# Optimization experiments

Measured on AMD Instinct MI355X. Metric: run time of the kernel, lower is better.

## Reference

```python
import jax, jax.numpy as jnp
import numpy as np

BETA = 0.9      # LIF leak factor
THR = 1.0       # firing threshold
SLOPE = 5.0     # surrogate-gradient sigmoid slope


def spike_fn(v):
    # Heaviside forward, sigmoid surrogate gradient (straight-through).
    hard = (v > THR).astype(v.dtype)
    surr = jax.nn.sigmoid(SLOPE * (v - THR))
    return hard + (surr - jax.lax.stop_gradient(surr))


def setup_inputs() -> dict:
    key = jax.random.key(0)
    ks = jax.random.split(key, 4)
    B, T, IN, H, OUT = 16, 128, 1024, 4096, 1024
    def lin_w(k, out_d, in_d):
        bound = 1.0 / np.sqrt(in_d)
        return jax.random.uniform(k, (out_d, in_d), jnp.float32, -bound, bound)
    return {
        "x": jax.random.normal(ks[0], (B, T, IN), jnp.float32),
        "w1": lin_w(ks[1], H, IN), "b1": jnp.zeros((H,), jnp.float32),
        "w2": lin_w(ks[2], H, H),  "b2": jnp.zeros((H,), jnp.float32),
        "w3": lin_w(ks[3], OUT, H), "b3": jnp.zeros((OUT,), jnp.float32),
    }


def reference(x, w1, b1, w2, b2, w3, b3):
    # x: [B, T, IN]; sequential per-timestep SNN feed-forward, readout = sum over time.
    B = x.shape[0]
    H = w1.shape[0]
    v0 = jnp.zeros((B, H), x.dtype)

    def step(carry, xt):                      # xt: [B, IN]
        v1, v2 = carry
        h1 = xt @ w1.T + b1                   # [B, H]
        v1 = BETA * v1 + h1
        s1 = spike_fn(v1)
        v1 = v1 - s1 * THR                    # soft reset
        h2 = s1 @ w2.T + b2                   # [B, H]
        v2 = BETA * v2 + h2
        s2 = spike_fn(v2)
        v2 = v2 - s2 * THR
        logits = s2 @ w3.T + b3               # [B, OUT]
        return (v1, v2), logits

    _, logits = jax.lax.scan(step, (v0, v0), jnp.swapaxes(x, 0, 1))  # [T, B, OUT]
    return logits.sum(axis=0)                 # readout_mode == 'sum'
```

## Files before the change

### kernel.cpp

```cpp
#include <hip/hip_runtime.h>
#include <hip/hip_bf16.h>

#define B_   16
#define T_   128
#define IN_  1024
#define H_   4096
#define OUT_ 1024
#define M_   (B_ * T_)

typedef __attribute__((ext_vector_type(8))) short short8;
typedef __attribute__((ext_vector_type(4))) float f32x4;
typedef __attribute__((ext_vector_type(4))) int i32x4;
typedef __attribute__((ext_vector_type(4))) unsigned short u16x4;
typedef unsigned short u16;
typedef signed char i8;

__device__ inline u16 f2bf_rne(float f) {
  unsigned u = __float_as_uint(f);
  unsigned r = u + 0x7FFFu + ((u >> 16) & 1u);
  return (u16)(r >> 16);
}
__device__ inline float bf2f(u16 s) {
  return __uint_as_float(((unsigned)s) << 16);
}
__device__ inline int pack4(int a, int b, int c, int d) {
  return (a & 255) | ((b & 255) << 8) | ((c & 255) << 16) | ((d & 255) << 24);
}

__device__ inline void xcd_swizzle(int bid0, int& bnI, int& bmI) {
  const int xcd = bid0 & 7;
  const int loc = bid0 >> 3;
  bnI = (xcd & 3) * 8 + (loc & 7);
  bmI = (xcd >> 2) * 8 + (loc >> 3);
}

#define NX_  (M_ * IN_)
#define NW1_ (H_ * IN_)
#define NW2_ (H_ * H_)

__device__ inline void split4bf(const float4 f, u16* __restrict__ hi,
                                u16* __restrict__ lo, size_t e) {
  u16x4 h, l;
  h.x = f2bf_rne(f.x); l.x = f2bf_rne(f.x - bf2f(h.x));
  h.y = f2bf_rne(f.y); l.y = f2bf_rne(f.y - bf2f(h.y));
  h.z = f2bf_rne(f.z); l.z = f2bf_rne(f.z - bf2f(h.z));
  h.w = f2bf_rne(f.w); l.w = f2bf_rne(f.w - bf2f(h.w));
  *(u16x4*)(hi + e) = h;
  *(u16x4*)(lo + e) = l;
}

__device__ inline void splitw2_1(float w, int& c0, int& c1, int& c2) {
  int wf = __float2int_rn(w * 268435456.0f);
  c0 = (wf + 32768) >> 16;
  int r0 = wf - (c0 << 16);
  if (r0 >= 32640) { c0 += 1; r0 -= 65536; }
  c1 = (r0 + 128) >> 8;
  c2 = r0 - (c1 << 8);
}

__global__ void split_xw1_kernel(const float4* __restrict__ x,
                                 const float4* __restrict__ w1,
                                 u16* __restrict__ xh, u16* __restrict__ xl,
                                 u16* __restrict__ w1h, u16* __restrict__ w1l) {
  const int total4 = (NX_ + NW1_) / 4;
  for (int i = blockIdx.x * blockDim.x + threadIdx.x; i < total4;
       i += gridDim.x * blockDim.x) {
    if (i < NX_ / 4) {
      split4bf(x[i], xh, xl, (size_t)i * 4);
    } else {
      int j = i - NX_ / 4;
      split4bf(w1[j], w1h, w1l, (size_t)j * 4);
    }
  }
}

#define BK1 64

__global__ __launch_bounds__(256, 2) void gemm1_rec(
    const u16* __restrict__ Ah, const u16* __restrict__ Al,
    const u16* __restrict__ Bh, const u16* __restrict__ Bl,
    const float* __restrict__ bias, i8* __restrict__ s1out,
    const float4* __restrict__ w2src,
    i8* __restrict__ p0, i8* __restrict__ p1, i8* __restrict__ p2) {
  __shared__ __align__(16) char smem[65536];
  u16* sAh = (u16*)smem;
  u16* sAl = (u16*)(smem + 16384);
  u16* sBh = (u16*)(smem + 32768);
  u16* sBl = (u16*)(smem + 49152);

  const int tid  = threadIdx.x;
  const int lane = tid & 63;
  const int wid  = tid >> 6;
  const int wm   = (wid >> 1) * 64;
  const int wn   = (wid & 1) * 64;
  const int bid  = blockIdx.y * 32 + blockIdx.x;
  int bnI, bmI;
  xcd_swizzle(bid, bnI, bmI);
  const int bm = bmI * 128;
  const int bn = bnI * 128;

  const int sdst = (tid & 7) * 8;
  const int scol = (((tid & 7) ^ ((tid >> 3) & 7)) * 8);
  const int q8   = (lane >> 4) * 8;
  const int rsw  = (lane & 7) * 8;

  f32x4 acc[4][4];
#pragma unroll
  for (int i = 0; i < 4; ++i)
#pragma unroll
    for (int j = 0; j < 4; ++j) acc[i][j] = (f32x4){0.f, 0.f, 0.f, 0.f};

  const int wbase = bid * 8192 + tid * 2;
  float4 wfa = w2src[wbase];
  float4 wfb = w2src[wbase + 1];

#pragma unroll 1
  for (int it = 0; it < IN_ / BK1; ++it) {
    const int kt = it * BK1;
    __syncthreads();
#pragma unroll
    for (int l = 0; l < 4; ++l) {
      int row = l * 32 + (tid >> 3);
      size_t ga = (size_t)(bm + row) * IN_ + kt + scol;
      size_t gb = (size_t)(bn + row) * IN_ + kt + scol;
      int ld = row * BK1 + sdst;
      __builtin_amdgcn_global_load_lds(
          (const __attribute__((address_space(1))) unsigned int*)(Ah + ga),
          (__attribute__((address_space(3))) unsigned int*)(&sAh[ld]), 16, 0, 0);
      __builtin_amdgcn_global_load_lds(
          (const __attribute__((address_space(1))) unsigned int*)(Al + ga),
          (__attribute__((address_space(3))) unsigned int*)(&sAl[ld]), 16, 0, 0);
      __builtin_amdgcn_global_load_lds(
          (const __attribute__((address_space(1))) unsigned int*)(Bh + gb),
          (__attribute__((address_space(3))) unsigned int*)(&sBh[ld]), 16, 0, 0);
      __builtin_amdgcn_global_load_lds(
          (const __attribute__((address_space(1))) unsigned int*)(Bl + gb),
          (__attribute__((address_space(3))) unsigned int*)(&sBl[ld]), 16, 0, 0);
    }
    __syncthreads();

    const int nit = (it + 1 < 16) ? it + 1 : 15;
    float4 nfa = w2src[wbase + nit * 512];
    float4 nfb = w2src[wbase + nit * 512 + 1];

    {
      const int sbase = bid * 8192 + it * 512 + tid * 2;
#pragma unroll
      for (int u = 0; u < 2; ++u) {
        float4 f = u ? wfb : wfa;
        int a0, a1, a2, b0, b1, b2, c0, c1, c2, d0, d1, d2;
        splitw2_1(f.x, a0, a1, a2);
        splitw2_1(f.y, b0, b1, b2);
        splitw2_1(f.z, c0, c1, c2);
        splitw2_1(f.w, d0, d1, d2);
        size_t e = (size_t)(sbase + u) * 4;
        *(int*)(p0 + e) = pack4(a0, b0, c0, d0);
        *(int*)(p1 + e) = pack4(a1, b1, c1, d1);
        *(int*)(p2 + e) = pack4(a2, b2, c2, d2);
      }
    }

#pragma unroll
    for (int ks = 0; ks < BK1; ks += 32) {
      const int swz = (ks + q8) ^ rsw;
      short8 ah[4], al[4], bh[4], bl[4];
#pragma unroll
      for (int i = 0; i < 4; ++i) {
        int ro = (wm + i * 16 + (lane & 15)) * BK1 + swz;
        ah[i] = *(const short8*)&sAh[ro];
        al[i] = *(const short8*)&sAl[ro];
      }
#pragma unroll
      for (int j = 0; j < 4; ++j) {
        int ro = (wn + j * 16 + (lane & 15)) * BK1 + swz;
        bh[j] = *(const short8*)&sBh[ro];
        bl[j] = *(const short8*)&sBl[ro];
      }
#pragma unroll
      for (int i = 0; i < 4; ++i)
#pragma unroll
        for (int j = 0; j < 4; ++j) {
          acc[i][j] = __builtin_amdgcn_mfma_f32_16x16x32_bf16(ah[i], bh[j], acc[i][j], 0, 0, 0);
          acc[i][j] = __builtin_amdgcn_mfma_f32_16x16x32_bf16(ah[i], bl[j], acc[i][j], 0, 0, 0);
          acc[i][j] = __builtin_amdgcn_mfma_f32_16x16x32_bf16(al[i], bh[j], acc[i][j], 0, 0, 0);
          acc[i][j] = __builtin_amdgcn_mfma_f32_16x16x32_bf16(al[i], bl[j], acc[i][j], 0, 0, 0);
        }
    }

    wfa = nfa;
    wfb = nfb;
  }

  float* hl = (float*)smem;
  const int c = tid & 127;
  const float bv = bias[bn + c];
  float v = 0.0f;
  __syncthreads();
#pragma unroll
  for (int half = 0; half < 2; ++half) {
    if (wm == half * 64) {
#pragma unroll
      for (int i = 0; i < 4; ++i)
#pragma unroll
        for (int j = 0; j < 4; ++j) {
          int col = wn + j * 16 + (lane & 15);
#pragma unroll
          for (int r = 0; r < 4; ++r) {
            int lrow = i * 16 + (lane >> 4) * 4 + r;
            hl[lrow * 128 + col] = acc[i][j][r];
          }
        }
    }
    __syncthreads();
    if (tid < 128) {
      for (int tt = 0; tt < 64; ++tt) {
        float h = hl[tt * 128 + c] + bv;
        v = 0.9f * v + h;
        i8 sp = 0;
        if (v > 1.0f) { sp = 1; v -= 1.0f; }
        s1out[(size_t)(bm + half * 64 + tt) * H_ + bn + c] = sp;
      }
    }
    __syncthreads();
  }
}

__global__ __launch_bounds__(256, 2) void gemm2_i8(
    const i8* __restrict__ A,
    const i8* __restrict__ P0, const i8* __restrict__ P1,
    const i8* __restrict__ P2,
    const float* __restrict__ bias, float* __restrict__ s2out) {
  __shared__ __align__(16) char smem[65536];
  i8* sA12 = (i8*)smem;
  i8* sB1  = (i8*)(smem + 16384);
  i8* sB2  = (i8*)(smem + 32768);
  i8* sA0  = (i8*)smem;
  i8* sB0  = (i8*)(smem + 32768);

  const int tid  = threadIdx.x;
  const int lane = tid & 63;
  const int wid  = tid >> 6;
  const int wm   = (wid >> 1) * 64;
  const int wn   = (wid & 1) * 64;
  const int bid  = blockIdx.y * 32 + blockIdx.x;
  int bnI, bmI;
  xcd_swizzle(bid, bnI, bmI);
  const int bm = bmI * 128;
  const int bn = bnI * 128;

  const int q16  = (lane >> 4) * 16;
  const int r15  = lane & 15;
  const int rswb = (lane & 7) * 16;

  f32x4 facc[4][4];

  {
    const int sdstB = (tid & 7) * 16;
    const int scolB = (((tid & 7) ^ ((tid >> 3) & 7)) * 16);
    i32x4 acc12[4][4];
#pragma unroll
    for (int i = 0; i < 4; ++i)
#pragma unroll
      for (int j = 0; j < 4; ++j) acc12[i][j] = (i32x4){0, 0, 0, 0};

#pragma unroll 1
    for (int kt = 0; kt < H_; kt += 128) {
      __syncthreads();
#pragma unroll
      for (int l = 0; l < 4; ++l) {
        int row = l * 32 + (tid >> 3);
        int ld  = row * 128 + sdstB;
        __builtin_amdgcn_global_load_lds(
            (const __attribute__((address_space(1))) unsigned int*)(A + (size_t)(bm + row) * H_ + kt + scolB),
            (__attribute__((address_space(3))) unsigned int*)(sA12 + ld), 16, 0, 0);
        __builtin_amdgcn_global_load_lds(
            (const __attribute__((address_space(1))) unsigned int*)(P1 + (size_t)(bn + row) * H_ + kt + scolB),
            (__attribute__((address_space(3))) unsigned int*)(sB1 + ld), 16, 0, 0);
        __builtin_amdgcn_global_load_lds(
            (const __attribute__((address_space(1))) unsigned int*)(P2 + (size_t)(bn + row) * H_ + kt + scolB),
            (__attribute__((address_space(3))) unsigned int*)(sB2 + ld), 16, 0, 0);
      }
      __syncthreads();

      i32x4 t[4][4];
#pragma unroll
      for (int i = 0; i < 4; ++i)
#pragma unroll
        for (int j = 0; j < 4; ++j) t[i][j] = (i32x4){0, 0, 0, 0};

#pragma unroll
      for (int ks = 0; ks < 2; ++ks) {
        const int swz = (ks * 64 + q16) ^ rswb;
        i32x4 a[4], b1[4], b2[4];
#pragma unroll
        for (int i = 0; i < 4; ++i)
          a[i] = *(const i32x4*)(sA12 + (wm + i * 16 + r15) * 128 + swz);
#pragma unroll
        for (int j = 0; j < 4; ++j) {
          int ro = (wn + j * 16 + r15) * 128 + swz;
          b1[j] = *(const i32x4*)(sB1 + ro);
          b2[j] = *(const i32x4*)(sB2 + ro);
        }
#pragma unroll
        for (int i = 0; i < 4; ++i)
#pragma unroll
          for (int j = 0; j < 4; ++j) {
            t[i][j]     = __builtin_amdgcn_mfma_i32_16x16x64_i8(a[i], b1[j], t[i][j], 0, 0, 0);
            acc12[i][j] = __builtin_amdgcn_mfma_i32_16x16x64_i8(a[i], b2[j], acc12[i][j], 0, 0, 0);
          }
      }
#pragma unroll
      for (int i = 0; i < 4; ++i)
#pragma unroll
        for (int j = 0; j < 4; ++j)
#pragma unroll
          for (int r = 0; r < 4; ++r)
            acc12[i][j][r] += t[i][j][r] << 8;
    }
#pragma unroll
    for (int i = 0; i < 4; ++i)
#pragma unroll
      for (int j = 0; j < 4; ++j)
#pragma unroll
        for (int r = 0; r < 4; ++r)
          facc[i][j][r] = 0x1p-28f * (float)acc12[i][j][r];
  }

  {
    const int strow = tid >> 4;
    const int sslot = tid & 15;
    i32x4 acc0[4][4];
#pragma unroll
    for (int i = 0; i < 4; ++i)
#pragma unroll
      for (int j = 0; j < 4; ++j) acc0[i][j] = (i32x4){0, 0, 0, 0};

#pragma unroll 1
    for (int kt = 0; kt < H_; kt += 256) {
      __syncthreads();
#pragma unroll
      for (int l = 0; l < 8; ++l) {
        int row = l * 16 + strow;
        int sc  = (sslot ^ (row & 15)) * 16;
        __builtin_amdgcn_global_load_lds(
            (const __attribute__((address_space(1))) unsigned int*)(A + (size_t)(bm + row) * H_ + kt + sc),
            (__attribute__((address_space(3))) unsigned int*)(sA0 + row * 256 + sslot * 16), 16, 0, 0);
        __builtin_amdgcn_global_load_lds(
            (const __attribute__((address_space(1))) unsigned int*)(P0 + (size_t)(bn + row) * H_ + kt + sc),
            (__attribute__((address_space(3))) unsigned int*)(sB0 + row * 256 + sslot * 16), 16, 0, 0);
      }
      __syncthreads();

#pragma unroll
      for (int ksi = 0; ksi < 4; ++ksi) {
        const int swz = (((ksi << 2) + (lane >> 4)) ^ r15) * 16;
        i32x4 a[4], b[4];
#pragma unroll
        for (int i = 0; i < 4; ++i)
          a[i] = *(const i32x4*)(sA0 + (wm + i * 16 + r15) * 256 + swz);
#pragma unroll
        for (int j = 0; j < 4; ++j)
          b[j] = *(const i32x4*)(sB0 + (wn + j * 16 + r15) * 256 + swz);
#pragma unroll
        for (int i = 0; i < 4; ++i)
#pragma unroll
          for (int j = 0; j < 4; ++j)
            acc0[i][j] = __builtin_amdgcn_mfma_i32_16x16x64_i8(a[i], b[j], acc0[i][j], 0, 0, 0);
      }
    }
#pragma unroll
    for (int i = 0; i < 4; ++i)
#pragma unroll
      for (int j = 0; j < 4; ++j)
#pragma unroll
        for (int r = 0; r < 4; ++r)
          facc[i][j][r] += 0x1p-12f * (float)acc0[i][j][r];
  }

  float* hl = (float*)smem;
  const int c = tid & 127;
  const float bv = bias[bn + c];
  float v = 0.0f, cnt = 0.0f;
  __syncthreads();
#pragma unroll
  for (int half = 0; half < 2; ++half) {
    if (wm == half * 64) {
#pragma unroll
      for (int i = 0; i < 4; ++i)
#pragma unroll
        for (int j = 0; j < 4; ++j) {
          int col = wn + j * 16 + (lane & 15);
#pragma unroll
          for (int r = 0; r < 4; ++r) {
            int lrow = i * 16 + (lane >> 4) * 4 + r;
            hl[lrow * 128 + col] = facc[i][j][r];
          }
        }
    }
    __syncthreads();
    if (tid < 128) {
      for (int tt = 0; tt < 64; ++tt) {
        float h = hl[tt * 128 + c] + bv;
        v = 0.9f * v + h;
        if (v > 1.0f) { cnt += 1.0f; v -= 1.0f; }
      }
    }
    __syncthreads();
  }
  if (tid < 128) s2out[(size_t)bmI * H_ + bn + c] = cnt;
}

__global__ void out_gemm_kernel(const float* __restrict__ s2sum,
                                const float* __restrict__ w3,
                                const float* __restrict__ b3,
                                float* __restrict__ out) {
  int o = blockIdx.x;
  int lane = threadIdx.x;
  float acc[B_];
#pragma unroll
  for (int b = 0; b < B_; ++b) acc[b] = 0.f;
  const float* wrow = w3 + (size_t)o * H_;
  for (int i = 0; i < H_ / 64; ++i) {
    float w = wrow[i * 64 + lane];
#pragma unroll
    for (int b = 0; b < B_; ++b)
      acc[b] += w * s2sum[b * H_ + i * 64 + lane];
  }
#pragma unroll
  for (int b = 0; b < B_; ++b) {
    float v = acc[b];
#pragma unroll
    for (int off = 32; off > 0; off >>= 1) v += __shfl_xor(v, off);
    if (lane == b) out[b * OUT_ + o] = v + (float)T_ * b3[o];
  }
}

extern "C" void kernel_launch(void* const* d_in, const int* in_sizes, int n_in,
                              void* d_out, int out_size, void* d_ws, size_t ws_size,
                              hipStream_t stream) {
  const float* x  = (const float*)d_in[0];
  const float* w1 = (const float*)d_in[1];
  const float* b1 = (const float*)d_in[2];
  const float* w2 = (const float*)d_in[3];
  const float* b2 = (const float*)d_in[4];
  const float* w3 = (const float*)d_in[5];
  const float* b3 = (const float*)d_in[6];
  float* out = (float*)d_out;

  char* ws = (char*)d_ws;
  i8*    s1    = (i8*)(ws);
  u16*   x_hi  = (u16*)(ws + 8388608);
  u16*   x_lo  = (u16*)(ws + 12582912);
  u16*   w1_hi = (u16*)(ws + 16777216);
  u16*   w1_lo = (u16*)(ws + 25165824);
  i8*    w2p0  = (i8*)(ws + 33554432);
  i8*    w2p1  = (i8*)(ws + 50331648);
  i8*    w2p2  = (i8*)(ws + 67108864);
  float* s2sum = (float*)(ws + 83886080);

  split_xw1_kernel<<<1024, 256, 0, stream>>>((const float4*)x, (const float4*)w1,
                                             x_hi, x_lo, w1_hi, w1_lo);

  dim3 g1(H_ / 128, M_ / 128);
  gemm1_rec<<<g1, 256, 0, stream>>>(x_hi, x_lo, w1_hi, w1_lo, b1, s1,
                                    (const float4*)w2, w2p0, w2p1, w2p2);

  gemm2_i8<<<g1, 256, 0, stream>>>(s1, w2p0, w2p1, w2p2, b2, s2sum);

  out_gemm_kernel<<<OUT_, 64, 0, stream>>>(s2sum, w3, b3, out);
}
```

Baseline: 174.4 us.

## Restructure int8 gemm2 into single-pass 256x128 tiles with double-buffered LDS pipeline

Replaces the two sequential K passes (P1/P2 then P0) with one fused K loop that loads A once and reuses it against all three weight planes. Tiles grow to 256x128 with 512 threads, and a double-buffered global_load_lds pipeline uses explicit vmcnt waits, split barriers and s_setprio around the MFMA bursts. The goal is to cut A reloads and hide global latency behind MFMA work. In exchange it holds three accumulator sets (more VGPRs), uses 80KB of LDS, and relies on hand-placed waitcnts, which makes correctness and occupancy fragile.

Result: no change. 174.8 us (+0.2%).

```diff
diff --git a/kernel.cpp b/kernel.cpp
--- a/kernel.cpp
+++ b/kernel.cpp
@@ -225,189 +225,171 @@
   }
 }
 
-__global__ __launch_bounds__(256, 2) void gemm2_i8(
+#define G2_OFFP1 16384
+#define G2_OFFP2 24576
+#define G2_OFFP0 32768
+#define G2_BUFS  40960
+
+#define G2_GLD(srcp, ldsp)                                                  \
+  __builtin_amdgcn_global_load_lds(                                         \
+      (const __attribute__((address_space(1))) unsigned int*)(srcp),        \
+      (__attribute__((address_space(3))) unsigned int*)(ldsp), 16, 0, 0)
+
+__global__ __launch_bounds__(512, 2) void gemm2_i8(
     const i8* __restrict__ A,
     const i8* __restrict__ P0, const i8* __restrict__ P1,
     const i8* __restrict__ P2,
     const float* __restrict__ bias, float* __restrict__ s2out) {
-  __shared__ __align__(16) char smem[65536];
-  i8* sA12 = (i8*)smem;
-  i8* sB1  = (i8*)(smem + 16384);
-  i8* sB2  = (i8*)(smem + 32768);
-  i8* sA0  = (i8*)smem;
-  i8* sB0  = (i8*)(smem + 32768);
+  __shared__ __align__(16) char smem[81920];
 
   const int tid  = threadIdx.x;
   const int lane = tid & 63;
   const int wid  = tid >> 6;
   const int wm   = (wid >> 1) * 64;
   const int wn   = (wid & 1) * 64;
-  const int bid  = blockIdx.y * 32 + blockIdx.x;
-  int bnI, bmI;
-  xcd_swizzle(bid, bnI, bmI);
-  const int bm = bmI * 128;
-  const int bn = bnI * 128;
-
-  const int q16  = (lane >> 4) * 16;
-  const int r15  = lane & 15;
-  const int rswb = (lane & 7) * 16;
-
-  f32x4 facc[4][4];
-
-  {
-    const int sdstB = (tid & 7) * 16;
-    const int scolB = (((tid & 7) ^ ((tid >> 3) & 7)) * 16);
-    i32x4 acc12[4][4];
+
+  const int bid = blockIdx.x;
+  const int xcd = bid & 7, loc = bid >> 3;
+  const int bmI = (xcd & 3) * 2 + (loc & 1);
+  const int bnI = (xcd >> 2) * 16 + (loc >> 1);
+  const int bm = bmI * 256, bn = bnI * 128;
+
+  const int j8   = tid & 7;
+  const int r8   = tid >> 3;
+  const int cc   = j8 ^ (r8 & 7);
+  const int srow = 2 * r8 + (cc >> 2);
+  const int scol = (cc & 3) * 16;
+  const int dst0 = r8 * 128 + j8 * 16;
+  const size_t gA = (size_t)(bm + srow) * H_ + scol;
+  const size_t gP = (size_t)(bn + srow) * H_ + scol;
+
+  const int r15 = lane & 15, qk = lane >> 4;
+  const int lro = (r15 >> 1) * 128 +
+                  (((((r15 & 1) << 2) + qk) ^ ((r15 >> 1) & 7)) * 16);
+  const int abase = wm * 64 + lro;
+  const int bbase = wn * 64 + lro;
+
+  i32x4 acc0[4][4], acc1[4][4], acc2[4][4];
+#pragma unroll
+  for (int i = 0; i < 4; ++i)
+#pragma unroll
+    for (int j = 0; j < 4; ++j) {
+      acc0[i][j] = (i32x4){0, 0, 0, 0};
+      acc1[i][j] = (i32x4){0, 0, 0, 0};
+      acc2[i][j] = (i32x4){0, 0, 0, 0};
+    }
+
+  G2_GLD(A + gA, smem + dst0);
+  G2_GLD(A + gA + (size_t)128 * H_, smem + 8192 + dst0);
+  G2_GLD(P1 + gP, smem + G2_OFFP1 + dst0);
+  G2_GLD(P2 + gP, smem + G2_OFFP2 + dst0);
+  G2_GLD(P0 + gP, smem + G2_OFFP0 + dst0);
+  G2_GLD(A + gA + 64, smem + G2_BUFS + dst0);
+  G2_GLD(A + gA + (size_t)128 * H_ + 64, smem + G2_BUFS + 8192 + dst0);
+  G2_GLD(P1 + gP + 64, smem + G2_BUFS + G2_OFFP1 + dst0);
+  asm volatile("s_waitcnt vmcnt(5)" ::: "memory");
+  __builtin_amdgcn_s_barrier();
+
+#pragma unroll 1
+  for (int t = 0; t < 64; ++t) {
+    char* cur = smem + (t & 1) * G2_BUFS;
+    char* nxt = smem + ((t + 1) & 1) * G2_BUFS;
+    const int kt1 = (t < 63 ? t + 1 : 63) << 6;
+    const int kt2 = (t < 62 ? t + 2 : 63) << 6;
+
+    i32x4 a[4], b[4];
+
 #pragma unroll
     for (int i = 0; i < 4; ++i)
-#pragma unroll
-      for (int j = 0; j < 4; ++j) acc12[i][j] = (i32x4){0, 0, 0, 0};
-
-#pragma unroll 1
-    for (int kt = 0; kt < H_; kt += 128) {
+      a[i] = *(const i32x4*)(cur + abase + i * 1024);
+#pragma unroll
+    for (int j = 0; j < 4; ++j)
+      b[j] = *(const i32x4*)(cur + G2_OFFP1 + bbase + j * 1024);
+    G2_GLD(P2 + gP + kt1, nxt + G2_OFFP2 + dst0);
+    G2_GLD(P0 + gP + kt1, nxt + G2_OFFP0 + dst0);
+    __builtin_amdgcn_s_barrier();
+    asm volatile("s_waitcnt lgkmcnt(0)" ::: "memory");
+    __builtin_amdgcn_s_setprio(1);
+#pragma unroll
+    for (int i = 0; i < 4; ++i)
+#pragma unroll
+      for (int j = 0; j < 4; ++j)
+        acc1[i][j] = __builtin_amdgcn_mfma_i32_16x16x64_i8(a[i], b[j], acc1[i][j], 0, 0, 0);
+    __builtin_amdgcn_s_setprio(0);
+    asm volatile("s_waitcnt vmcnt(5)" ::: "memory");
+    __builtin_amdgcn_s_barrier();
+
+#pragma unroll
+    for (int j = 0; j < 4; ++j)
+      b[j] = *(const i32x4*)(cur + G2_OFFP2 + bbase + j * 1024);
+    G2_GLD(A + gA + kt2, cur + dst0);
+    G2_GLD(A + gA + (size_t)128 * H_ + kt2, cur + 8192 + dst0);
+    G2_GLD(P1 + gP + kt2, cur + G2_OFFP1 + dst0);
+    __builtin_amdgcn_s_barrier();
+    asm volatile("s_waitcnt lgkmcnt(0)" ::: "memory");
+    __builtin_amdgcn_s_setprio(1);
+#pragma unroll
+    for (int i = 0; i < 4; ++i)
+#pragma unroll
+      for (int j = 0; j < 4; ++j)
+        acc2[i][j] = __builtin_amdgcn_mfma_i32_16x16x64_i8(a[i], b[j], acc2[i][j], 0, 0, 0);
+    __builtin_amdgcn_s_setprio(0);
+    __builtin_amdgcn_s_barrier();
+
+#pragma unroll
+    for (int j = 0; j < 4; ++j)
+      b[j] = *(const i32x4*)(cur + G2_OFFP0 + bbase + j * 1024);
+    __builtin_amdgcn_s_barrier();
+    asm volatile("s_waitcnt lgkmcnt(0)" ::: "memory");
+    __builtin_amdgcn_s_setprio(1);
+#pragma unroll
+    for (int i = 0; i < 4; ++i)
+#pragma unroll
+      for (int j = 0; j < 4; ++j)
+        acc0[i][j] = __builtin_amdgcn_mfma_i32_16x16x64_i8(a[i], b[j], acc0[i][j], 0, 0, 0);
+    __builtin_amdgcn_s_setprio(0);
+    asm volatile("s_waitcnt vmcnt(5)" ::: "memory");
+    __builtin_amdgcn_s_barrier();
+  }
+
+  float* hl = (float*)smem;
+  const int ec = tid & 127;
+  const float bv = bias[bn + ec];
+  asm volatile("s_waitcnt vmcnt(0)" ::: "memory");
+  __syncthreads();
+#pragma unroll
+  for (int hb = 0; hb < 2; ++hb) {
+    float v = 0.0f, cnt = 0.0f;
+#pragma unroll
+    for (int half = 0; half < 2; ++half) {
+      const int hq = hb * 2 + half;
+      if (wm == hq * 64) {
+#pragma unroll
+        for (int i = 0; i < 4; ++i)
+#pragma unroll
+          for (int j = 0; j < 4; ++j) {
+            int col = wn + j * 16 + (lane & 15);
+#pragma unroll
+            for (int r = 0; r < 4; ++r) {
+              int lrow = i * 16 + (lane >> 4) * 4 + r;
+              float val = 0x1p-28f * (float)((acc1[i][j][r] << 8) + acc2[i][j][r]) +
+                          0x1p-12f * (float)acc0[i][j][r];
+              hl[lrow * 128 + col] = val;
+            }
+          }
+      }
       __syncthreads();
-#pragma unroll
-      for (int l = 0; l < 4; ++l) {
-        int row = l * 32 + (tid >> 3);
-        int ld  = row * 128 + sdstB;
-        __builtin_amdgcn_global_load_lds(
-            (const __attribute__((address_space(1))) unsigned int*)(A + (size_t)(bm + row) * H_ + kt + scolB),
-            (__attribute__((address_space(3))) unsigned int*)(sA12 + ld), 16, 0, 0);
-        __builtin_amdgcn_global_load_lds(
-            (const __attribute__((address_space(1))) unsigned int*)(P1 + (size_t)(bn + row) * H_ + kt + scolB),
-            (__attribute__((address_space(3))) unsigned int*)(sB1 + ld), 16, 0, 0);
-        __builtin_amdgcn_global_load_lds(
-            (const __attribute__((address_space(1))) unsigned int*)(P2 + (size_t)(bn + row) * H_ + kt + scolB),
-            (__attribute__((address_space(3))) unsigned int*)(sB2 + ld), 16, 0, 0);
+      if (tid < 128) {
+        for (int tt = 0; tt < 64; ++tt) {
+          float h = hl[tt * 128 + ec] + bv;
+          v = 0.9f * v + h;
+          if (v > 1.0f) { cnt += 1.0f; v -= 1.0f; }
+        }
       }
       __syncthreads();
-
-      i32x4 t[4][4];
-#pragma unroll
-      for (int i = 0; i < 4; ++i)
-#pragma unroll
-        for (int j = 0; j < 4; ++j) t[i][j] = (i32x4){0, 0, 0, 0};
-
-#pragma unroll
-      for (int ks = 0; ks < 2; ++ks) {
-        const int swz = (ks * 64 + q16) ^ rswb;
-        i32x4 a[4], b1[4], b2[4];
-#pragma unroll
-        for (int i = 0; i < 4; ++i)
-          a[i] = *(const i32x4*)(sA12 + (wm + i * 16 + r15) * 128 + swz);
-#pragma unroll
-        for (int j = 0; j < 4; ++j) {
-          int ro = (wn + j * 16 + r15) * 128 + swz;
-          b1[j] = *(const i32x4*)(sB1 + ro);
-          b2[j] = *(const i32x4*)(sB2 + ro);
-        }
-#pragma unroll
-        for (int i = 0; i < 4; ++i)
-#pragma unroll
-          for (int j = 0; j < 4; ++j) {
-            t[i][j]     = __builtin_amdgcn_mfma_i32_16x16x64_i8(a[i], b1[j], t[i][j], 0, 0, 0);
-            acc12[i][j] = __builtin_amdgcn_mfma_i32_16x16x64_i8(a[i], b2[j], acc12[i][j], 0, 0, 0);
-          }
-      }
-#pragma unroll
-      for (int i = 0; i < 4; ++i)
-#pragma unroll
-        for (int j = 0; j < 4; ++j)
-#pragma unroll
-          for (int r = 0; r < 4; ++r)
-            acc12[i][j][r] += t[i][j][r] << 8;
-    }
-#pragma unroll
-    for (int i = 0; i < 4; ++i)
-#pragma unroll
-      for (int j = 0; j < 4; ++j)
-#pragma unroll
-        for (int r = 0; r < 4; ++r)
-          facc[i][j][r] = 0x1p-28f * (float)acc12[i][j][r];
-  }
-
-  {
-    const int strow = tid >> 4;
-    const int sslot = tid & 15;
-    i32x4 acc0[4][4];
-#pragma unroll
-    for (int i = 0; i < 4; ++i)
-#pragma unroll
-      for (int j = 0; j < 4; ++j) acc0[i][j] = (i32x4){0, 0, 0, 0};
-
-#pragma unroll 1
-    for (int kt = 0; kt < H_; kt += 256) {
-      __syncthreads();
-#pragma unroll
-      for (int l = 0; l < 8; ++l) {
-        int row = l * 16 + strow;
-        int sc  = (sslot ^ (row & 15)) * 16;
-        __builtin_amdgcn_global_load_lds(
-            (const __attribute__((address_space(1))) unsigned int*)(A + (size_t)(bm + row) * H_ + kt + sc),
-            (__attribute__((address_space(3))) unsigned int*)(sA0 + row * 256 + sslot * 16), 16, 0, 0);
-        __builtin_amdgcn_global_load_lds(
-            (const __attribute__((address_space(1))) unsigned int*)(P0 + (size_t)(bn + row) * H_ + kt + sc),
-            (__attribute__((address_space(3))) unsigned int*)(sB0 + row * 256 + sslot * 16), 16, 0, 0);
-      }
-      __syncthreads();
-
-#pragma unroll
-      for (int ksi = 0; ksi < 4; ++ksi) {
-        const int swz = (((ksi << 2) + (lane >> 4)) ^ r15) * 16;
-        i32x4 a[4], b[4];
-#pragma unroll
-        for (int i = 0; i < 4; ++i)
-          a[i] = *(const i32x4*)(sA0 + (wm + i * 16 + r15) * 256 + swz);
-#pragma unroll
-        for (int j = 0; j < 4; ++j)
-          b[j] = *(const i32x4*)(sB0 + (wn + j * 16 + r15) * 256 + swz);
-#pragma unroll
-        for (int i = 0; i < 4; ++i)
-#pragma unroll
-          for (int j = 0; j < 4; ++j)
-            acc0[i][j] = __builtin_amdgcn_mfma_i32_16x16x64_i8(a[i], b[j], acc0[i][j], 0, 0, 0);
-      }
-    }
-#pragma unroll
-    for (int i = 0; i < 4; ++i)
-#pragma unroll
-      for (int j = 0; j < 4; ++j)
-#pragma unroll
-        for (int r = 0; r < 4; ++r)
-          facc[i][j][r] += 0x1p-12f * (float)acc0[i][j][r];
-  }
-
-  float* hl = (float*)smem;
-  const int c = tid & 127;
-  const float bv = bias[bn + c];
-  float v = 0.0f, cnt = 0.0f;
-  __syncthreads();
-#pragma unroll
-  for (int half = 0; half < 2; ++half) {
-    if (wm == half * 64) {
-#pragma unroll
-      for (int i = 0; i < 4; ++i)
-#pragma unroll
-        for (int j = 0; j < 4; ++j) {
-          int col = wn + j * 16 + (lane & 15);
-#pragma unroll
-          for (int r = 0; r < 4; ++r) {
-            int lrow = i * 16 + (lane >> 4) * 4 + r;
-            hl[lrow * 128 + col] = facc[i][j][r];
-          }
-        }
-    }
-    __syncthreads();
-    if (tid < 128) {
-      for (int tt = 0; tt < 64; ++tt) {
-        float h = hl[tt * 128 + c] + bv;
-        v = 0.9f * v + h;
-        if (v > 1.0f) { cnt += 1.0f; v -= 1.0f; }
-      }
-    }
-    __syncthreads();
-  }
-  if (tid < 128) s2out[(size_t)bmI * H_ + bn + c] = cnt;
+    }
+    if (tid < 128) s2out[(size_t)(2 * bmI + hb) * H_ + bn + ec] = cnt;
+  }
 }
 
 __global__ void out_gemm_kernel(const float* __restrict__ s2sum,
@@ -465,7 +447,7 @@
   gemm1_rec<<<g1, 256, 0, stream>>>(x_hi, x_lo, w1_hi, w1_lo, b1, s1,
                                     (const float4*)w2, w2p0, w2p1, w2p2);
 
-  gemm2_i8<<<g1, 256, 0, stream>>>(s1, w2p0, w2p1, w2p2, b2, s2sum);
+  gemm2_i8<<<dim3(256), 512, 0, stream>>>(s1, w2p0, w2p1, w2p2, b2, s2sum);
 
   out_gemm_kernel<<<OUT_, 64, 0, stream>>>(s2sum, w3, b3, out);
 }
```

## Load gemm2 A operand directly to registers and halve LDS footprint

Applied to the files above, without the earlier changes.

The spike-matrix A operand in gemm2 is now read straight from global memory into registers instead of being staged through LDS. This cuts LDS to 32 KB and removes the A-side LDS writes and reads. The cross-product accumulation now keeps two separate accumulator sets (acc1, acc2) and combines them once at the end, instead of shifting and adding every k-tile. The P0 pass now uses 128-wide k tiles with the same swizzle as the other pass, and s_setprio is raised around the MFMA blocks. Costs are higher register pressure from the extra accumulators and per-lane global loads that are less coalesced, which could hurt occupancy or add latency.

After: 247.7 us. 42.0% more time.

```diff
diff --git a/kernel.cpp b/kernel.cpp
--- a/kernel.cpp
+++ b/kernel.cpp
@@ -225,17 +225,20 @@
   }
 }
 
+#define G2_GLD(srcp, ldsp)                                                  \
+  __builtin_amdgcn_global_load_lds(                                         \
+      (const __attribute__((address_space(1))) unsigned int*)(srcp),        \
+      (__attribute__((address_space(3))) unsigned int*)(ldsp), 16, 0, 0)
+
 __global__ __launch_bounds__(256, 2) void gemm2_i8(
     const i8* __restrict__ A,
     const i8* __restrict__ P0, const i8* __restrict__ P1,
     const i8* __restrict__ P2,
     const float* __restrict__ bias, float* __restrict__ s2out) {
-  __shared__ __align__(16) char smem[65536];
-  i8* sA12 = (i8*)smem;
-  i8* sB1  = (i8*)(smem + 16384);
-  i8* sB2  = (i8*)(smem + 32768);
-  i8* sA0  = (i8*)smem;
-  i8* sB0  = (i8*)(smem + 32768);
+  __shared__ __align__(16) char smem[32768];
+  i8* sB1 = (i8*)smem;
+  i8* sB2 = (i8*)(smem + 16384);
+  i8* sB0 = (i8*)smem;
 
   const int tid  = threadIdx.x;
   const int lane = tid & 63;
@@ -252,16 +255,22 @@
   const int r15  = lane & 15;
   const int rswb = (lane & 7) * 16;
 
+  const int sdstB = (tid & 7) * 16;
+  const int scolB = (((tid & 7) ^ ((tid >> 3) & 7)) * 16);
+
+  const size_t aBase = (size_t)(bm + wm + r15) * H_ + q16;
+
   f32x4 facc[4][4];
 
   {
-    const int sdstB = (tid & 7) * 16;
-    const int scolB = (((tid & 7) ^ ((tid >> 3) & 7)) * 16);
-    i32x4 acc12[4][4];
+    i32x4 acc1[4][4], acc2[4][4];
 #pragma unroll
     for (int i = 0; i < 4; ++i)
 #pragma unroll
-      for (int j = 0; j < 4; ++j) acc12[i][j] = (i32x4){0, 0, 0, 0};
+      for (int j = 0; j < 4; ++j) {
+        acc1[i][j] = (i32x4){0, 0, 0, 0};
+        acc2[i][j] = (i32x4){0, 0, 0, 0};
+      }
 
 #pragma unroll 1
     for (int kt = 0; kt < H_; kt += 128) {
@@ -270,102 +279,86 @@
       for (int l = 0; l < 4; ++l) {
         int row = l * 32 + (tid >> 3);
         int ld  = row * 128 + sdstB;
-        __builtin_amdgcn_global_load_lds(
-            (const __attribute__((address_space(1))) unsigned int*)(A + (size_t)(bm + row) * H_ + kt + scolB),
-            (__attribute__((address_space(3))) unsigned int*)(sA12 + ld), 16, 0, 0);
-        __builtin_amdgcn_global_load_lds(
-            (const __attribute__((address_space(1))) unsigned int*)(P1 + (size_t)(bn + row) * H_ + kt + scolB),
-            (__attribute__((address_space(3))) unsigned int*)(sB1 + ld), 16, 0, 0);
-        __builtin_amdgcn_global_load_lds(
-            (const __attribute__((address_space(1))) unsigned int*)(P2 + (size_t)(bn + row) * H_ + kt + scolB),
-            (__attribute__((address_space(3))) unsigned int*)(sB2 + ld), 16, 0, 0);
-      }
+        G2_GLD(P1 + (size_t)(bn + row) * H_ + kt + scolB, sB1 + ld);
+        G2_GLD(P2 + (size_t)(bn + row) * H_ + kt + scolB, sB2 + ld);
+      }
+      i32x4 a[2][4];
+#pragma unroll
+      for (int ks = 0; ks < 2; ++ks)
+#pragma unroll
+        for (int i = 0; i < 4; ++i)
+          a[ks][i] = *(const i32x4*)(A + aBase + (size_t)i * 16 * H_ + kt + ks * 64);
       __syncthreads();
-
-      i32x4 t[4][4];
-#pragma unroll
-      for (int i = 0; i < 4; ++i)
-#pragma unroll
-        for (int j = 0; j < 4; ++j) t[i][j] = (i32x4){0, 0, 0, 0};
 
 #pragma unroll
       for (int ks = 0; ks < 2; ++ks) {
         const int swz = (ks * 64 + q16) ^ rswb;
-        i32x4 a[4], b1[4], b2[4];
-#pragma unroll
-        for (int i = 0; i < 4; ++i)
-          a[i] = *(const i32x4*)(sA12 + (wm + i * 16 + r15) * 128 + swz);
+        i32x4 b1[4], b2[4];
 #pragma unroll
         for (int j = 0; j < 4; ++j) {
           int ro = (wn + j * 16 + r15) * 128 + swz;
           b1[j] = *(const i32x4*)(sB1 + ro);
           b2[j] = *(const i32x4*)(sB2 + ro);
         }
+        __builtin_amdgcn_s_setprio(1);
 #pragma unroll
         for (int i = 0; i < 4; ++i)
 #pragma unroll
           for (int j = 0; j < 4; ++j) {
-            t[i][j]     = __builtin_amdgcn_mfma_i32_16x16x64_i8(a[i], b1[j], t[i][j], 0, 0, 0);
-            acc12[i][j] = __builtin_amdgcn_mfma_i32_16x16x64_i8(a[i], b2[j], acc12[i][j], 0, 0, 0);
+            acc1[i][j] = __builtin_amdgcn_mfma_i32_16x16x64_i8(a[ks][i], b1[j], acc1[i][j], 0, 0, 0);
+            acc2[i][j] = __builtin_amdgcn_mfma_i32_16x16x64_i8(a[ks][i], b2[j], acc2[i][j], 0, 0, 0);
           }
-      }
-#pragma unroll
-      for (int i = 0; i < 4; ++i)
+        __builtin_amdgcn_s_setprio(0);
+      }
+    }
+
+#pragma unroll
+    for (int i = 0; i < 4; ++i)
+#pragma unroll
+      for (int j = 0; j < 4; ++j)
+#pragma unroll
+        for (int r = 0; r < 4; ++r)
+          facc[i][j][r] = 0x1p-28f * (float)((acc1[i][j][r] << 8) + acc2[i][j][r]);
+  }
+
+  {
+    i32x4 acc0[4][4];
+#pragma unroll
+    for (int i = 0; i < 4; ++i)
+#pragma unroll
+      for (int j = 0; j < 4; ++j) acc0[i][j] = (i32x4){0, 0, 0, 0};
+
+#pragma unroll 1
+    for (int kt = 0; kt < H_; kt += 128) {
+      __syncthreads();
+#pragma unroll
+      for (int l = 0; l < 4; ++l) {
+        int row = l * 32 + (tid >> 3);
+        int ld  = row * 128 + sdstB;
+        G2_GLD(P0 + (size_t)(bn + row) * H_ + kt + scolB, sB0 + ld);
+      }
+      i32x4 a[2][4];
+#pragma unroll
+      for (int ks = 0; ks < 2; ++ks)
+#pragma unroll
+        for (int i = 0; i < 4; ++i)
+          a[ks][i] = *(const i32x4*)(A + aBase + (size_t)i * 16 * H_ + kt + ks * 64);
+      __syncthreads();
+
+#pragma unroll
+      for (int ks = 0; ks < 2; ++ks) {
+        const int swz = (ks * 64 + q16) ^ rswb;
+        i32x4 b[4];
 #pragma unroll
         for (int j = 0; j < 4; ++j)
-#pragma unroll
-          for (int r = 0; r < 4; ++r)
-            acc12[i][j][r] += t[i][j][r] << 8;
-    }
-#pragma unroll
-    for (int i = 0; i < 4; ++i)
-#pragma unroll
-      for (int j = 0; j < 4; ++j)
-#pragma unroll
-        for (int r = 0; r < 4; ++r)
-          facc[i][j][r] = 0x1p-28f * (float)acc12[i][j][r];
-  }
-
-  {
-    const int strow = tid >> 4;
-    const int sslot = tid & 15;
-    i32x4 acc0[4][4];
-#pragma unroll
-    for (int i = 0; i < 4; ++i)
-#pragma unroll
-      for (int j = 0; j < 4; ++j) acc0[i][j] = (i32x4){0, 0, 0, 0};
-
-#pragma unroll 1
-    for (int kt = 0; kt < H_; kt += 256) {
-      __syncthreads();
-#pragma unroll
-      for (int l = 0; l < 8; ++l) {
-        int row = l * 16 + strow;
-        int sc  = (sslot ^ (row & 15)) * 16;
-        __builtin_amdgcn_global_load_lds(
-            (const __attribute__((address_space(1))) unsigned int*)(A + (size_t)(bm + row) * H_ + kt + sc),
-            (__attribute__((address_space(3))) unsigned int*)(sA0 + row * 256 + sslot * 16), 16, 0, 0);
-        __builtin_amdgcn_global_load_lds(
-            (const __attribute__((address_space(1))) unsigned int*)(P0 + (size_t)(bn + row) * H_ + kt + sc),
-            (__attribute__((address_space(3))) unsigned int*)(sB0 + row * 256 + sslot * 16), 16, 0, 0);
-      }
-      __syncthreads();
-
-#pragma unroll
-      for (int ksi = 0; ksi < 4; ++ksi) {
-        const int swz = (((ksi << 2) + (lane >> 4)) ^ r15) * 16;
-        i32x4 a[4], b[4];
+          b[j] = *(const i32x4*)(sB0 + (wn + j * 16 + r15) * 128 + swz);
+        __builtin_amdgcn_s_setprio(1);
 #pragma unroll
         for (int i = 0; i < 4; ++i)
-          a[i] = *(const i32x4*)(sA0 + (wm + i * 16 + r15) * 256 + swz);
-#pragma unroll
-        for (int j = 0; j < 4; ++j)
-          b[j] = *(const i32x4*)(sB0 + (wn + j * 16 + r15) * 256 + swz);
-#pragma unroll
-        for (int i = 0; i < 4; ++i)
 #pragma unroll
           for (int j = 0; j < 4; ++j)
-            acc0[i][j] = __builtin_amdgcn_mfma_i32_16x16x64_i8(a[i], b[j], acc0[i][j], 0, 0, 0);
+            acc0[i][j] = __builtin_amdgcn_mfma_i32_16x16x64_i8(a[ks][i], b[j], acc0[i][j], 0, 0, 0);
+        __builtin_amdgcn_s_setprio(0);
       }
     }
 #pragma unroll
```
